# Optimization experiments

Measured on AMD Instinct MI355X. Metric: run time of the kernel, lower is better.

## Reference

```python
import jax, jax.numpy as jnp
import numpy as np

B, IN, H = 4096, 512, 1024
ALPHA, RHO = 0.001, 0.05

def setup_inputs() -> dict:
    key = jax.random.key(0)
    ks = jax.random.split(key, 9)
    inp = jax.random.normal(ks[0], (B, IN), dtype=jnp.float32)
    time = jax.random.uniform(ks[1], (B, 1), dtype=jnp.float32) * 100.0
    hx = jax.random.normal(ks[2], (B, H), dtype=jnp.float32)
    cx = jax.random.normal(ks[3], (B, H), dtype=jnp.float32)
    # params (match torch init scales loosely)
    Wxh_w = jax.random.normal(ks[4], (4 * H, IN), dtype=jnp.float32) / np.sqrt(IN)
    Wxh_b = jnp.zeros((4 * H,), dtype=jnp.float32)
    Whh_w = jax.random.normal(ks[5], (4 * H, H), dtype=jnp.float32) / np.sqrt(H)
    tau = jax.random.normal(ks[6], (H,), dtype=jnp.float32) * 0.5 + 5.0
    s = jax.random.uniform(ks[7], (H,), dtype=jnp.float32) * tau
    alpha = jnp.array([ALPHA], dtype=jnp.float32)
    rho = jnp.array([RHO], dtype=jnp.float32)
    return {"input": inp, "time": time, "hx": hx, "cx": cx,
            "Wxh_w": Wxh_w, "Wxh_b": Wxh_b, "Whh_w": Whh_w,
            "tau": tau, "s": s, "alpha": alpha, "rho": rho}

def _time_gate(time, s, tau, alpha, rho):
    # phi: [B, H] (time [B,1] broadcast against s/tau [H])
    phi = jnp.fmod(time - s, tau) / tau
    k = jnp.where(phi < rho / 2.0, 2.0 * phi / rho,
        jnp.where(phi < rho, 2.0 - 2.0 * phi / rho, alpha * phi))
    # computed under torch.no_grad() in the original
    return jax.lax.stop_gradient(k)

def reference(input, time, hx, cx, Wxh_w, Wxh_b, Whh_w, tau, s, alpha, rho):
    gates = input @ Wxh_w.T + Wxh_b + hx @ Whh_w.T  # [B, 4H]
    i, f, g, o = jnp.split(gates, 4, axis=1)
    k = _time_gate(time, s, tau, alpha, rho)
    ft = jax.nn.sigmoid(f + 1.0 - k)
    it = jax.nn.sigmoid(i) * k
    gt = jnp.tanh(g) * k
    ot = jax.nn.sigmoid(o) * k
    cy = ft * cx + it * gt
    hy = ot * jnp.tanh(cy)
    return (hy, cy)
```

## Files before the change

kernel.cpp:

```cpp
#include <hip/hip_runtime.h>

#define AS1 __attribute__((address_space(1)))
#define AS3 __attribute__((address_space(3)))

typedef _Float16 half_t;
typedef __attribute__((ext_vector_type(8))) _Float16 f16x8;
typedef __attribute__((ext_vector_type(4))) float f32x4;

static constexpr int Bsz = 4096;
static constexpr int INs = 512;
static constexpr int Hs  = 1024;
static constexpr int BM  = 128;
static constexpr int BH  = 32;
static constexpr int BK  = 64;
static constexpr int NIT = INs / BK + Hs / BK;

static constexpr size_t XN  = (size_t)Bsz * INs;
static constexpr size_t HXN = (size_t)Bsz * Hs;
static constexpr size_t WXN = (size_t)4 * Hs * INs;
static constexpr size_t WHN = (size_t)4 * Hs * Hs;
static constexpr size_t OFF_X  = 0;
static constexpr size_t OFF_HX = XN;
static constexpr size_t OFF_WX = XN + HXN;
static constexpr size_t OFF_WH = XN + HXN + WXN;
static constexpr size_t TOT    = XN + HXN + WXN + WHN;

__device__ __forceinline__ float sigm(float x) {
  return 1.0f / (1.0f + __expf(-x));
}
__device__ __forceinline__ float tanh_fast(float x) {
  const float e = __expf(2.0f * x);
  return 1.0f - 2.0f / (e + 1.0f);
}

__global__ __launch_bounds__(256)
void cvt_kernel(const float* __restrict__ x, const float* __restrict__ hx,
                const float* __restrict__ wx, const float* __restrict__ wh,
                half_t* __restrict__ ws) {
  const size_t cid = (size_t)blockIdx.x * 256 + threadIdx.x;
  const size_t e = cid * 8;
  const float* src; size_t off;
  if (e < OFF_HX)      { src = x;  off = e - OFF_X; }
  else if (e < OFF_WX) { src = hx; off = e - OFF_HX; }
  else if (e < OFF_WH) { src = wx; off = e - OFF_WX; }
  else                 { src = wh; off = e - OFF_WH; }
  const f32x4 a = *(const f32x4*)(src + off);
  const f32x4 b = *(const f32x4*)(src + off + 4);
  f16x8 o;
  o[0]=(half_t)a[0]; o[1]=(half_t)a[1]; o[2]=(half_t)a[2]; o[3]=(half_t)a[3];
  o[4]=(half_t)b[0]; o[5]=(half_t)b[1]; o[6]=(half_t)b[2]; o[7]=(half_t)b[3];
  *(f16x8*)(ws + e) = o;
}

__global__ __launch_bounds__(256, 2)
void plstm_gemm(const half_t* __restrict__ xin,
                const half_t* __restrict__ hxp,
                const float* __restrict__ cxp,
                const half_t* __restrict__ wxh,
                const float* __restrict__ biasp,
                const half_t* __restrict__ whh,
                const float* __restrict__ timep,
                const float* __restrict__ taup,
                const float* __restrict__ sp,
                const float* __restrict__ alphap,
                const float* __restrict__ rhop,
                float* __restrict__ outp)
{
  __shared__ half_t As[2][BM * BK];
  __shared__ half_t Bs[2][BM * BK];

  const int tid  = threadIdx.x;
  const int w    = tid >> 6;
  const int lane = tid & 63;
  const int l15  = lane & 15;
  const int grp  = lane >> 4;
  const int wr   = w >> 1;
  const int wc   = w & 1;

  const int wg = blockIdx.x + (blockIdx.y << 5);
  const int xk = wg & 7;
  const int q  = wg >> 3;
  const int m0 = (q >> 2) * BM;
  const int h0 = ((xk << 2) + (q & 3)) * BH;

  f32x4 acc[4][4] = {};

  const int ldr = tid >> 3;
  const int ldc = tid & 7;

  auto stage = [&](int t, int p) {
    const bool p1 = t >= INs / BK;
    const half_t* Ap = p1 ? hxp : xin;
    const half_t* Wp = p1 ? whh : wxh;
    const int Ka = p1 ? Hs : INs;
    const int k0 = (p1 ? (t - INs / BK) : t) * BK;
    #pragma unroll
    for (int i = 0; i < 4; ++i) {
      const int e    = i * 32 + ldr;
      const int gc8  = ldc ^ (e & 7);
      const int wrow = ((e >> 4) & 3) * Hs + h0 + ((e >> 6) << 4) + (e & 15);
      const half_t* ga = Ap + (size_t)(m0 + e) * Ka + (k0 + gc8 * 8);
      __builtin_amdgcn_global_load_lds((AS1 void*)ga,
          (AS3 void*)(As[p] + (e * 8 + ldc) * 8), 16, 0, 0);
      const half_t* gw = Wp + (size_t)wrow * Ka + (k0 + gc8 * 8);
      __builtin_amdgcn_global_load_lds((AS1 void*)gw,
          (AS3 void*)(Bs[p] + (e * 8 + ldc) * 8), 16, 0, 0);
    }
  };

  auto compute = [&](int p) {
    #pragma unroll
    for (int kk = 0; kk < 2; ++kk) {
      const int c8x = kk * 4 + grp;
      f16x8 af[4], bfr[4];
      #pragma unroll
      for (int mt = 0; mt < 4; ++mt) {
        const int e = wr * 64 + mt * 16 + l15;
        af[mt] = *(const f16x8*)(As[p] + (e * 8 + (c8x ^ (l15 & 7))) * 8);
      }
      #pragma unroll
      for (int nt = 0; nt < 4; ++nt) {
        const int e = wc * 64 + nt * 16 + l15;
        bfr[nt] = *(const f16x8*)(Bs[p] + (e * 8 + (c8x ^ (l15 & 7))) * 8);
      }
      #pragma unroll
      for (int mt = 0; mt < 4; ++mt)
        #pragma unroll
        for (int nt = 0; nt < 4; ++nt)
          acc[mt][nt] = __builtin_amdgcn_mfma_f32_16x16x32_f16(
              af[mt], bfr[nt], acc[mt][nt], 0, 0, 0);
    }
  };

  stage(0, 0);
  __syncthreads();

  #pragma unroll 1
  for (int it = 0; it < NIT - 1; ++it) {
    stage(it + 1, (it + 1) & 1);
    compute(it & 1);
    __syncthreads();
  }
  compute((NIT - 1) & 1);

  const int h = h0 + wc * 16 + l15;
  const float bi  = biasp[h];
  const float bfv = biasp[Hs + h];
  const float bg  = biasp[2 * Hs + h];
  const float bo  = biasp[3 * Hs + h];
  const float sv = sp[h], tauv = taup[h];
  const float alphav = alphap[0], rhov = rhop[0], rh = 0.5f * rhov;
  const float rtau   = 1.0f / tauv;
  const float tworho = 2.0f / rhov;

  #pragma unroll
  for (int mt = 0; mt < 4; ++mt) {
    const f32x4 t4 = *(const f32x4*)(timep + m0 + wr * 64 + mt * 16 + grp * 4);
    #pragma unroll
    for (int r = 0; r < 4; ++r) {
      const int brow = m0 + wr * 64 + mt * 16 + grp * 4 + r;
      const float qv  = (t4[r] - sv) * rtau;
      const float phi = qv - truncf(qv);
      const float kv  = phi < rh   ? phi * tworho
                      : (phi < rhov ? 2.0f - phi * tworho
                                    : alphav * phi);

      const float iv = acc[mt][0][r] + bi;
      const float fv = acc[mt][1][r] + bfv;
      const float gv = acc[mt][2][r] + bg;
      const float ov = acc[mt][3][r] + bo;
      const float cxv = cxp[(size_t)brow * Hs + h];
      const float ft = sigm(fv + 1.0f - kv);
      const float it2 = sigm(iv) * kv;
      const float gt = tanh_fast(gv) * kv;
      const float ot = sigm(ov) * kv;
      const float cy = ft * cxv + it2 * gt;
      const float hy = ot * tanh_fast(cy);

      outp[(size_t)brow * Hs + h] = hy;
      outp[(size_t)Bsz * Hs + (size_t)brow * Hs + h] = cy;
    }
  }
}

__global__ __launch_bounds__(256, 3)
void plstm_gemm_f32(const float* __restrict__ xin, const float* __restrict__ timep,
                    const float* __restrict__ hxp, const float* __restrict__ cxp,
                    const float* __restrict__ wxh, const float* __restrict__ biasp,
                    const float* __restrict__ whh, const float* __restrict__ taup,
                    const float* __restrict__ sp, const float* __restrict__ alphap,
                    const float* __restrict__ rhop, float* __restrict__ outp)
{
  __shared__ half_t As[BM * BK];
  __shared__ half_t Bsf[BM * BK];

  const int tid  = threadIdx.x;
  const int w    = tid >> 6;
  const int lane = tid & 63;
  const int l15  = lane & 15;
  const int grp  = lane >> 4;
  const int wr   = w >> 1;
  const int wc   = w & 1;

  const int m0 = blockIdx.x * BM;
  const int h0 = blockIdx.y * BH;

  f32x4 acc[4][4] = {};
  const int ldr = tid >> 3;
  const int ldc = tid & 7;

  for (int it = 0; it < NIT; ++it) {
    const bool p1 = it >= INs / BK;
    const float* Ap = p1 ? hxp : xin;
    const float* Wp = p1 ? whh : wxh;
    const int Ka = p1 ? Hs : INs;
    const int k0 = (p1 ? (it - INs / BK) : it) * BK;
    #pragma unroll
    for (int i = 0; i < 4; ++i) {
      const int e    = i * 32 + ldr;
      const int gc8  = ldc ^ (e & 7);
      const int wrow = ((e >> 4) & 3) * Hs + h0 + ((e >> 6) << 4) + (e & 15);
      const float* ga = Ap + (size_t)(m0 + e) * Ka + (k0 + gc8 * 8);
      const f32x4 a0v = *(const f32x4*)ga, a1v = *(const f32x4*)(ga + 4);
      f16x8 pa;
      pa[0]=(half_t)a0v[0]; pa[1]=(half_t)a0v[1]; pa[2]=(half_t)a0v[2]; pa[3]=(half_t)a0v[3];
      pa[4]=(half_t)a1v[0]; pa[5]=(half_t)a1v[1]; pa[6]=(half_t)a1v[2]; pa[7]=(half_t)a1v[3];
      *(f16x8*)(As + (e * 8 + ldc) * 8) = pa;
      const float* gw = Wp + (size_t)wrow * Ka + (k0 + gc8 * 8);
      const f32x4 b0v = *(const f32x4*)gw, b1v = *(const f32x4*)(gw + 4);
      f16x8 pb;
      pb[0]=(half_t)b0v[0]; pb[1]=(half_t)b0v[1]; pb[2]=(half_t)b0v[2]; pb[3]=(half_t)b0v[3];
      pb[4]=(half_t)b1v[0]; pb[5]=(half_t)b1v[1]; pb[6]=(half_t)b1v[2]; pb[7]=(half_t)b1v[3];
      *(f16x8*)(Bsf + (e * 8 + ldc) * 8) = pb;
    }
    __syncthreads();
    #pragma unroll
    for (int kk = 0; kk < 2; ++kk) {
      const int c8x = kk * 4 + grp;
      f16x8 af[4], bfr[4];
      #pragma unroll
      for (int mt = 0; mt < 4; ++mt) {
        const int e = wr * 64 + mt * 16 + l15;
        af[mt] = *(const f16x8*)(As + (e * 8 + (c8x ^ (l15 & 7))) * 8);
      }
      #pragma unroll
      for (int nt = 0; nt < 4; ++nt) {
        const int e = wc * 64 + nt * 16 + l15;
        bfr[nt] = *(const f16x8*)(Bsf + (e * 8 + (c8x ^ (l15 & 7))) * 8);
      }
      #pragma unroll
      for (int mt = 0; mt < 4; ++mt)
        #pragma unroll
        for (int nt = 0; nt < 4; ++nt)
          acc[mt][nt] = __builtin_amdgcn_mfma_f32_16x16x32_f16(
              af[mt], bfr[nt], acc[mt][nt], 0, 0, 0);
    }
    __syncthreads();
  }

  const int h = h0 + wc * 16 + l15;
  const float bi  = biasp[h];
  const float bfv = biasp[Hs + h];
  const float bg  = biasp[2 * Hs + h];
  const float bo  = biasp[3 * Hs + h];
  const float sv = sp[h], tauv = taup[h];
  const float alphav = alphap[0], rhov = rhop[0], rh = 0.5f * rhov;
  const float rtau   = 1.0f / tauv;
  const float tworho = 2.0f / rhov;

  #pragma unroll
  for (int mt = 0; mt < 4; ++mt) {
    const f32x4 t4 = *(const f32x4*)(timep + m0 + wr * 64 + mt * 16 + grp * 4);
    #pragma unroll
    for (int r = 0; r < 4; ++r) {
      const int brow = m0 + wr * 64 + mt * 16 + grp * 4 + r;
      const float qv  = (t4[r] - sv) * rtau;
      const float phi = qv - truncf(qv);
      const float kv  = phi < rh   ? phi * tworho
                      : (phi < rhov ? 2.0f - phi * tworho
                                    : alphav * phi);
      const float iv = acc[mt][0][r] + bi;
      const float fv = acc[mt][1][r] + bfv;
      const float gv = acc[mt][2][r] + bg;
      const float ov = acc[mt][3][r] + bo;
      const float cxv = cxp[(size_t)brow * Hs + h];
      const float ft = sigm(fv + 1.0f - kv);
      const float it2 = sigm(iv) * kv;
      const float gt = tanh_fast(gv) * kv;
      const float ot = sigm(ov) * kv;
      const float cy = ft * cxv + it2 * gt;
      const float hy = ot * tanh_fast(cy);
      outp[(size_t)brow * Hs + h] = hy;
      outp[(size_t)Bsz * Hs + (size_t)brow * Hs + h] = cy;
    }
  }
}

extern "C" void kernel_launch(void* const* d_in, const int* in_sizes, int n_in,
                              void* d_out, int out_size, void* d_ws, size_t ws_size,
                              hipStream_t stream) {
  (void)in_sizes; (void)n_in; (void)out_size;
  const float* xin   = (const float*)d_in[0];
  const float* timep = (const float*)d_in[1];
  const float* hxp   = (const float*)d_in[2];
  const float* cxp   = (const float*)d_in[3];
  const float* wxh   = (const float*)d_in[4];
  const float* biasp = (const float*)d_in[5];
  const float* whh   = (const float*)d_in[6];
  const float* taup  = (const float*)d_in[7];
  const float* sp    = (const float*)d_in[8];
  const float* alphap= (const float*)d_in[9];
  const float* rhop  = (const float*)d_in[10];
  float* outp = (float*)d_out;

  dim3 grid(Bsz / BM, Hs / BH);
  if (ws_size >= TOT * sizeof(half_t)) {
    half_t* ws = (half_t*)d_ws;
    cvt_kernel<<<(int)(TOT / 8 / 256), 256, 0, stream>>>(xin, hxp, wxh, whh, ws);
    plstm_gemm<<<grid, 256, 0, stream>>>(
        ws + OFF_X, ws + OFF_HX, cxp, ws + OFF_WX, biasp, ws + OFF_WH,
        timep, taup, sp, alphap, rhop, outp);
  } else {
    plstm_gemm_f32<<<grid, 256, 0, stream>>>(
        xin, timep, hxp, cxp, wxh, biasp, whh,
        taup, sp, alphap, rhop, outp);
  }
}
```

Before: 197.3 us.

## Halve K tile to 32 with new LDS swizzle and raise occupancy to 4

```diff
diff --git a/kernel.cpp b/kernel.cpp
--- a/kernel.cpp
+++ b/kernel.cpp
@@ -12,8 +12,8 @@
 static constexpr int Hs  = 1024;
 static constexpr int BM  = 128;
 static constexpr int BH  = 32;
-static constexpr int BK  = 64;
-static constexpr int NIT = INs / BK + Hs / BK;
+static constexpr int BK2 = 32;
+static constexpr int NIT2 = INs / BK2 + Hs / BK2;
 
 static constexpr size_t XN  = (size_t)Bsz * INs;
 static constexpr size_t HXN = (size_t)Bsz * Hs;
@@ -52,7 +52,7 @@
   *(f16x8*)(ws + e) = o;
 }
 
-__global__ __launch_bounds__(256, 2)
+__global__ __launch_bounds__(256, 4)
 void plstm_gemm(const half_t* __restrict__ xin,
                 const half_t* __restrict__ hxp,
                 const float* __restrict__ cxp,
@@ -66,8 +66,8 @@
                 const float* __restrict__ rhop,
                 float* __restrict__ outp)
 {
-  __shared__ half_t As[2][BM * BK];
-  __shared__ half_t Bs[2][BM * BK];
+  __shared__ half_t As[2][BM * BK2];
+  __shared__ half_t Bs[2][BM * BK2];
 
   const int tid  = threadIdx.x;
   const int w    = tid >> 6;
@@ -85,63 +85,61 @@
 
   f32x4 acc[4][4] = {};
 
-  const int ldr = tid >> 3;
-  const int ldc = tid & 7;
+  const int sr  = tid >> 2;
+  const int sc  = tid & 3;
+  const int swz = (tid >> 4) & 3;
+  const int gcA = sc ^ swz;
 
   auto stage = [&](int t, int p) {
-    const bool p1 = t >= INs / BK;
+    const bool p1 = t >= INs / BK2;
     const half_t* Ap = p1 ? hxp : xin;
     const half_t* Wp = p1 ? whh : wxh;
     const int Ka = p1 ? Hs : INs;
-    const int k0 = (p1 ? (t - INs / BK) : t) * BK;
-    #pragma unroll
-    for (int i = 0; i < 4; ++i) {
-      const int e    = i * 32 + ldr;
-      const int gc8  = ldc ^ (e & 7);
+    const int k0 = (p1 ? (t - INs / BK2) : t) * BK2;
+    #pragma unroll
+    for (int i = 0; i < 2; ++i) {
+      const int e    = i * 64 + sr;
       const int wrow = ((e >> 4) & 3) * Hs + h0 + ((e >> 6) << 4) + (e & 15);
-      const half_t* ga = Ap + (size_t)(m0 + e) * Ka + (k0 + gc8 * 8);
+      const half_t* ga = Ap + (size_t)(m0 + e) * Ka + (k0 + gcA * 8);
       __builtin_amdgcn_global_load_lds((AS1 void*)ga,
-          (AS3 void*)(As[p] + (e * 8 + ldc) * 8), 16, 0, 0);
-      const half_t* gw = Wp + (size_t)wrow * Ka + (k0 + gc8 * 8);
+          (AS3 void*)(As[p] + e * 32 + sc * 8), 16, 0, 0);
+      const half_t* gw = Wp + (size_t)wrow * Ka + (k0 + gcA * 8);
       __builtin_amdgcn_global_load_lds((AS1 void*)gw,
-          (AS3 void*)(Bs[p] + (e * 8 + ldc) * 8), 16, 0, 0);
+          (AS3 void*)(Bs[p] + e * 32 + sc * 8), 16, 0, 0);
     }
   };
 
   auto compute = [&](int p) {
-    #pragma unroll
-    for (int kk = 0; kk < 2; ++kk) {
-      const int c8x = kk * 4 + grp;
-      f16x8 af[4], bfr[4];
+    const int cs = (l15 >> 2) & 3;
+    f16x8 af[4], bfr[4];
+    #pragma unroll
+    for (int mt = 0; mt < 4; ++mt) {
+      const int e = wr * 64 + mt * 16 + l15;
+      af[mt] = *(const f16x8*)(As[p] + e * 32 + ((grp ^ cs) * 8));
+    }
+    #pragma unroll
+    for (int nt = 0; nt < 4; ++nt) {
+      const int e = wc * 64 + nt * 16 + l15;
+      bfr[nt] = *(const f16x8*)(Bs[p] + e * 32 + ((grp ^ cs) * 8));
+    }
+    #pragma unroll
+    for (int mt = 0; mt < 4; ++mt)
       #pragma unroll
-      for (int mt = 0; mt < 4; ++mt) {
-        const int e = wr * 64 + mt * 16 + l15;
-        af[mt] = *(const f16x8*)(As[p] + (e * 8 + (c8x ^ (l15 & 7))) * 8);
-      }
-      #pragma unroll
-      for (int nt = 0; nt < 4; ++nt) {
-        const int e = wc * 64 + nt * 16 + l15;
-        bfr[nt] = *(const f16x8*)(Bs[p] + (e * 8 + (c8x ^ (l15 & 7))) * 8);
-      }
-      #pragma unroll
-      for (int mt = 0; mt < 4; ++mt)
-        #pragma unroll
-        for (int nt = 0; nt < 4; ++nt)
-          acc[mt][nt] = __builtin_amdgcn_mfma_f32_16x16x32_f16(
-              af[mt], bfr[nt], acc[mt][nt], 0, 0, 0);
-    }
+      for (int nt = 0; nt < 4; ++nt)
+        acc[mt][nt] = __builtin_amdgcn_mfma_f32_16x16x32_f16(
+            af[mt], bfr[nt], acc[mt][nt], 0, 0, 0);
   };
 
   stage(0, 0);
   __syncthreads();
 
   #pragma unroll 1
-  for (int it = 0; it < NIT - 1; ++it) {
-    stage(it + 1, (it + 1) & 1);
-    compute(it & 1);
+  for (int t = 0; t < NIT2 - 1; ++t) {
+    stage(t + 1, (t + 1) & 1);
+    compute(t & 1);
     __syncthreads();
   }
-  compute((NIT - 1) & 1);
+  compute((NIT2 - 1) & 1);
 
   const int h = h0 + wc * 16 + l15;
   const float bi  = biasp[h];
@@ -191,8 +189,8 @@
                     const float* __restrict__ sp, const float* __restrict__ alphap,
                     const float* __restrict__ rhop, float* __restrict__ outp)
 {
-  __shared__ half_t As[BM * BK];
-  __shared__ half_t Bsf[BM * BK];
+  __shared__ half_t As[BM * 64];
+  __shared__ half_t Bsf[BM * 64];
 
   const int tid  = threadIdx.x;
   const int w    = tid >> 6;
@@ -208,13 +206,14 @@
   f32x4 acc[4][4] = {};
   const int ldr = tid >> 3;
   const int ldc = tid & 7;
+  const int NIT = INs / 64 + Hs / 64;
 
   for (int it = 0; it < NIT; ++it) {
-    const bool p1 = it >= INs / BK;
+    const bool p1 = it >= INs / 64;
     const float* Ap = p1 ? hxp : xin;
     const float* Wp = p1 ? whh : wxh;
     const int Ka = p1 ? Hs : INs;
-    const int k0 = (p1 ? (it - INs / BK) : it) * BK;
+    const int k0 = (p1 ? (it - INs / 64) : it) * 64;
     #pragma unroll
     for (int i = 0; i < 4; ++i) {
       const int e    = i * 32 + ldr;
```

Result: faster. 192.9 us (-2.2%).
